# Optimization experiments

Measured on AMD Instinct MI355X. Metric: run time of the kernel, lower is better.

Reference implementation:

```python
import jax, jax.numpy as jnp
import numpy as np

B, S, IN = 32, 512, 19
DE, DD = 256, 128      # encoder / decoder d_model
HE, HD = 8, 4          # heads
LE, LD = 6, 2          # layers
FE, FD = 4 * DE, 4 * DD
EPS = 1e-5


def _ln(x, g, b):
    m = x.mean(-1, keepdims=True)
    v = ((x - m) ** 2).mean(-1, keepdims=True)
    return (x - m) / jnp.sqrt(v + EPS) * g + b


def _mha(x, qkv_w, qkv_b, out_w, out_b, kpad, nh):
    Bq, Sq, D = x.shape
    dh = D // nh
    qkv = x @ qkv_w.T + qkv_b
    q, k, v = jnp.split(qkv, 3, axis=-1)
    hs = lambda t: t.reshape(Bq, Sq, nh, dh).transpose(0, 2, 1, 3)  # -> [B,h,S,dh]
    q, k, v = hs(q), hs(k), hs(v)
    scores = jnp.einsum('bhqd,bhkd->bhqk', q, k) / float(np.sqrt(dh))
    scores = jnp.where(kpad[:, None, None, :], -1e9, scores)  # mask padded keys
    attn = jax.nn.softmax(scores, axis=-1)
    o = jnp.einsum('bhqk,bhkd->bhqd', attn, v).transpose(0, 2, 1, 3).reshape(Bq, Sq, D)
    return o @ out_w.T + out_b


def _block(x, p, kpad, nh):
    qkv_w, qkv_b, ow, ob, f1w, f1b, f2w, f2b, g1, b1, g2, b2 = p
    x = _ln(x + _mha(x, qkv_w, qkv_b, ow, ob, kpad, nh), g1, b1)
    h = jax.nn.relu(x @ f1w.T + f1b) @ f2w.T + f2b
    return _ln(x + h, g2, b2)


def _run(x, ps, kpad, nh, L):
    for i in range(L):
        x = _block(x, tuple(p[i] for p in ps), kpad, nh)
    return x


def _forward(event_tensor, w_in_enc, b_in_enc,
             enc_qkv_w, enc_qkv_b, enc_out_w, enc_out_b,
             enc_f1_w, enc_f1_b, enc_f2_w, enc_f2_b,
             enc_g1, enc_b1, enc_g2, enc_b2,
             mask_token, e2d_w,
             dec_qkv_w, dec_qkv_b, dec_out_w, dec_out_b,
             dec_f1_w, dec_f1_b, dec_f2_w, dec_f2_b,
             dec_g1, dec_b1, dec_g2, dec_b2,
             qh_w, qh_b, dth_w, dth_b,
             attention_mask, pred_mask):
    visible = attention_mask & (~pred_mask)
    counts = visible.sum(axis=1)                                  # [B]
    order = jnp.argsort(~visible, axis=1, stable=True)            # visible positions packed first, in order
    tok = event_tensor @ w_in_enc.T + b_in_enc                    # [B,S,DE]
    vis = jnp.take_along_axis(tok, order[:, :, None], axis=1)
    pos = jnp.arange(S)
    enc_pad = pos[None, :] >= counts[:, None]                      # True = padded slot
    vis = jnp.where(enc_pad[:, :, None], 0.0, vis)
    enc_ps = (enc_qkv_w, enc_qkv_b, enc_out_w, enc_out_b, enc_f1_w, enc_f1_b,
              enc_f2_w, enc_f2_b, enc_g1, enc_b1, enc_g2, enc_b2)
    enc_out = _run(vis, enc_ps, enc_pad, HE, LE)
    dec_vis = enc_out @ e2d_w.T                                    # [B,S,DD]
    idx = jnp.cumsum(visible.astype(jnp.int32), axis=1) - 1        # position -> packed index
    gathered = jnp.take_along_axis(dec_vis, jnp.clip(idx, 0)[:, :, None], axis=1)
    dec_in = jnp.where(visible[:, :, None], gathered, mask_token)  # mask token at masked/pad slots
    dec_ps = (dec_qkv_w, dec_qkv_b, dec_out_w, dec_out_b, dec_f1_w, dec_f1_b,
              dec_f2_w, dec_f2_b, dec_g1, dec_b1, dec_g2, dec_b2)
    dec_out = _run(dec_in, dec_ps, ~attention_mask, HD, LD)
    q = dec_out @ qh_w.T + qh_b
    dt = dec_out @ dth_w.T + dth_b
    return jnp.concatenate([q, dt], axis=-1)                       # [B,S,2]


def setup_inputs():
    key = jax.random.key(0)
    ks = iter(jax.random.split(key, 64))
    nrm = lambda shp, s=0.02: jax.random.normal(next(ks), shp, jnp.float32) * s
    d = {}
    d['event_tensor'] = jax.random.normal(next(ks), (B, S, IN), jnp.float32)
    lengths = jax.random.randint(next(ks), (B,), S // 2, S + 1)
    pos = jnp.arange(S)
    am = pos[None, :] < lengths[:, None]
    pm = (jax.random.uniform(next(ks), (B, S)) < 0.75) & am
    pm = pm.at[:, 0].set(False)  # guarantee >=1 visible token per row
    d['attention_mask'] = am
    d['pred_mask'] = pm
    d['w_in_enc'] = nrm((DE, IN)); d['b_in_enc'] = jnp.zeros((DE,), jnp.float32)
    d['enc_qkv_w'] = nrm((LE, 3 * DE, DE)); d['enc_qkv_b'] = jnp.zeros((LE, 3 * DE), jnp.float32)
    d['enc_out_w'] = nrm((LE, DE, DE));     d['enc_out_b'] = jnp.zeros((LE, DE), jnp.float32)
    d['enc_f1_w'] = nrm((LE, FE, DE));      d['enc_f1_b'] = jnp.zeros((LE, FE), jnp.float32)
    d['enc_f2_w'] = nrm((LE, DE, FE));      d['enc_f2_b'] = jnp.zeros((LE, DE), jnp.float32)
    d['enc_g1'] = jnp.ones((LE, DE), jnp.float32); d['enc_b1'] = jnp.zeros((LE, DE), jnp.float32)
    d['enc_g2'] = jnp.ones((LE, DE), jnp.float32); d['enc_b2'] = jnp.zeros((LE, DE), jnp.float32)
    d['mask_token'] = nrm((DD,))
    d['e2d_w'] = nrm((DD, DE))
    d['dec_qkv_w'] = nrm((LD, 3 * DD, DD)); d['dec_qkv_b'] = jnp.zeros((LD, 3 * DD), jnp.float32)
    d['dec_out_w'] = nrm((LD, DD, DD));     d['dec_out_b'] = jnp.zeros((LD, DD), jnp.float32)
    d['dec_f1_w'] = nrm((LD, FD, DD));      d['dec_f1_b'] = jnp.zeros((LD, FD), jnp.float32)
    d['dec_f2_w'] = nrm((LD, DD, FD));      d['dec_f2_b'] = jnp.zeros((LD, DD), jnp.float32)
    d['dec_g1'] = jnp.ones((LD, DD), jnp.float32); d['dec_b1'] = jnp.zeros((LD, DD), jnp.float32)
    d['dec_g2'] = jnp.ones((LD, DD), jnp.float32); d['dec_b2'] = jnp.zeros((LD, DD), jnp.float32)
    d['qh_w'] = nrm((1, DD));  d['qh_b'] = jnp.zeros((1,), jnp.float32)
    d['dth_w'] = nrm((1, DD)); d['dth_b'] = jnp.zeros((1,), jnp.float32)
    return d


def reference(event_tensor, attention_mask, pred_mask, w_in_enc, b_in_enc,
              enc_qkv_w, enc_qkv_b, enc_out_w, enc_out_b,
              enc_f1_w, enc_f1_b, enc_f2_w, enc_f2_b,
              enc_g1, enc_b1, enc_g2, enc_b2,
              mask_token, e2d_w,
              dec_qkv_w, dec_qkv_b, dec_out_w, dec_out_b,
              dec_f1_w, dec_f1_b, dec_f2_w, dec_f2_b,
              dec_g1, dec_b1, dec_g2, dec_b2,
              qh_w, qh_b, dth_w, dth_b):
    return _forward(event_tensor, w_in_enc, b_in_enc,
                    enc_qkv_w, enc_qkv_b, enc_out_w, enc_out_b,
                    enc_f1_w, enc_f1_b, enc_f2_w, enc_f2_b,
                    enc_g1, enc_b1, enc_g2, enc_b2,
                    mask_token, e2d_w,
                    dec_qkv_w, dec_qkv_b, dec_out_w, dec_out_b,
                    dec_f1_w, dec_f1_b, dec_f2_w, dec_f2_b,
                    dec_g1, dec_b1, dec_g2, dec_b2,
                    qh_w, qh_b, dth_w, dth_b,
                    attention_mask, pred_mask)
```

## Files before the change

### kernel.cpp

```cpp
#include <hip/hip_runtime.h>
#include <hip/hip_bf16.h>

#define B_ 32
#define S_ 512
#define IN_ 19
#define DE_ 256
#define DD_ 128
#define HE_ 8
#define HD_ 4
#define LE_ 6
#define LD_ 2
#define FE_ 1024
#define FD_ 512
#define DH_ 32

typedef __attribute__((ext_vector_type(8))) short short8;
typedef __attribute__((ext_vector_type(4))) float f32x4;

__device__ __forceinline__ short f2bf(float f) {
    union { float f; unsigned u; } x; x.f = f;
    unsigned r = x.u + 0x7fff + ((x.u >> 16) & 1);
    return (short)(r >> 16);
}
__device__ __forceinline__ float bf2f(short s) {
    union { unsigned u; float f; } x; x.u = ((unsigned)(unsigned short)s) << 16;
    return x.f;
}

#define GLL16(g, l) __builtin_amdgcn_global_load_lds( \
    (const __attribute__((address_space(1))) void*)(g), \
    (__attribute__((address_space(3))) void*)(l), 16, 0, 0)

#define QSCALE 0.2550653169f

#define NCONV 9
struct ConvTab {
    const float* src[NCONV];
    short* dst[NCONV];
    int len[NCONV];
};
__global__ __launch_bounds__(S_) void conv_plan_kernel(
    ConvTab tab, int total,
    const int* __restrict__ am, const int* __restrict__ pm,
    int* __restrict__ counts, int* __restrict__ lengths, int* __restrict__ order,
    int* __restrict__ visible, int* __restrict__ idx) {
    if (blockIdx.x < B_) {
        int b = blockIdx.x, s = threadIdx.x;
        __shared__ int sc[S_];
        int a = (am[b * S_ + s] != 0);
        int v = a && (pm[b * S_ + s] == 0);
        visible[b * S_ + s] = v;
        sc[s] = v | (a << 16);
        __syncthreads();
#pragma unroll
        for (int off = 1; off < S_; off <<= 1) {
            int t = (s >= off) ? sc[s - off] : 0;
            __syncthreads();
            sc[s] += t;
            __syncthreads();
        }
        int incl = sc[s] & 0xffff;
        int tot = sc[S_ - 1];
        int total2 = tot & 0xffff;
        if (s == 0) { counts[b] = total2; lengths[b] = tot >> 16; }
        idx[b * S_ + s] = (incl > 0) ? incl - 1 : 0;
        if (v) order[b * S_ + incl - 1] = s;
        else   order[b * S_ + total2 + (s - incl)] = s;
    } else {
        int i = (blockIdx.x - B_) * S_ + threadIdx.x;
        if (i >= total) return;
        int j = i;
        for (int e = 0; e < NCONV; ++e) {
            if (j < tab.len[e]) { tab.dst[e][j] = f2bf(tab.src[e][j]); return; }
            j -= tab.len[e];
        }
    }
}

__global__ __launch_bounds__(DE_) void enc_embed_kernel(
    const float* __restrict__ ev, const float* __restrict__ w, const float* __restrict__ bias,
    const int* __restrict__ counts, const int* __restrict__ order, short* __restrict__ out) {
    int bs = blockIdx.x;
    int b = bs / S_, s = bs % S_;
    int d = threadIdx.x;
    __shared__ float e[IN_];
    bool padded = (s >= counts[b]);
    int src = order[bs];
    if (threadIdx.x < IN_)
        e[threadIdx.x] = padded ? 0.f : ev[(size_t)(b * S_ + src) * IN_ + threadIdx.x];
    __syncthreads();
    float acc = bias[d];
#pragma unroll
    for (int i = 0; i < IN_; ++i) acc += e[i] * w[d * IN_ + i];
    out[(size_t)bs * DE_ + d] = padded ? f2bf(0.f) : f2bf(acc);
}

template <int TM, int TN, bool RELU, bool QKV>
__device__ __forceinline__ void gemm_lds_body(
    const short* __restrict__ A, const short* __restrict__ Wt, const float* __restrict__ bias,
    short* __restrict__ C, int N, int K,
    short* __restrict__ qb, short* __restrict__ kb, short* __restrict__ vtb, int H, int D,
    const int* __restrict__ live) {
    constexpr int HM = TM / 2, HN = TN / 2;
    constexpr int MI = HM / 16, NI = HN / 16;
    constexpr int NCHA = TM / 16, NCH = (TM + TN) / 16;
    int bm = blockIdx.y * TM, bn = blockIdx.x * TN;
    if (live && (bm & (S_ - 1)) >= live[bm >> 9]) return;
    __shared__ short As[2][TM][32];
    __shared__ short Bs[2][TN][32];
    int t = threadIdx.x;
    int wave = t >> 6, lane = t & 63;
    int wm = (wave >> 1) * HM, wn = (wave & 1) * HN;
    int c = lane & 15, quad = lane >> 4;
    f32x4 acc[MI][NI];
#pragma unroll
    for (int i = 0; i < MI; ++i)
#pragma unroll
        for (int j = 0; j < NI; ++j) acc[i][j] = (f32x4){0.f, 0.f, 0.f, 0.f};

    int srow = lane >> 2, scol = (lane & 3) * 8;
    int nk = K >> 5;

    auto stage = [&](int buf, int k0) {
#pragma unroll
        for (int ch0 = 0; ch0 < NCH; ch0 += 4) {
            int ch = ch0 + wave;
            if (ch < NCHA)
                GLL16(A + (size_t)(bm + ch * 16 + srow) * K + k0 + scol, &As[buf][ch * 16][0]);
            else if (ch < NCH)
                GLL16(Wt + (size_t)(bn + (ch - NCHA) * 16 + srow) * K + k0 + scol,
                      &Bs[buf][(ch - NCHA) * 16][0]);
        }
    };

    stage(0, 0);
    __syncthreads();
    for (int kt = 0; kt < nk; ++kt) {
        int cur = kt & 1;
        if (kt + 1 < nk) stage(cur ^ 1, (kt + 1) << 5);
        short8 av[MI], bv[NI];
#pragma unroll
        for (int mi = 0; mi < MI; ++mi) av[mi] = *(const short8*)&As[cur][wm + mi * 16 + c][quad * 8];
#pragma unroll
        for (int ni = 0; ni < NI; ++ni) bv[ni] = *(const short8*)&Bs[cur][wn + ni * 16 + c][quad * 8];
#pragma unroll
        for (int mi = 0; mi < MI; ++mi)
#pragma unroll
            for (int ni = 0; ni < NI; ++ni)
                acc[mi][ni] = __builtin_amdgcn_mfma_f32_16x16x32_bf16(av[mi], bv[ni], acc[mi][ni], 0, 0, 0);
        __syncthreads();
    }
#pragma unroll
    for (int mi = 0; mi < MI; ++mi)
#pragma unroll
        for (int ni = 0; ni < NI; ++ni)
#pragma unroll
            for (int r = 0; r < 4; ++r) {
                int R = bm + wm + mi * 16 + quad * 4 + r;
                int Ncol = bn + wn + ni * 16 + c;
                float v = acc[mi][ni][r] + (bias ? bias[Ncol] : 0.f);
                if (RELU) v = fmaxf(v, 0.f);
                if (!QKV) {
                    C[(size_t)R * N + Ncol] = f2bf(v);
                } else {
                    int s = R & (S_ - 1), b2 = R >> 9;
                    if (Ncol < D) {
                        int h = Ncol >> 5, d = Ncol & 31;
                        qb[(((size_t)b2 * H + h) * S_ + s) * DH_ + d] = f2bf(v * QSCALE);
                    } else if (Ncol < 2 * D) {
                        int n2 = Ncol - D, h = n2 >> 5, d = n2 & 31;
                        kb[(((size_t)b2 * H + h) * S_ + s) * DH_ + d] = f2bf(v);
                    } else {
                        int n2 = Ncol - 2 * D, h = n2 >> 5, d = n2 & 31;
                        vtb[(((size_t)b2 * H + h) * DH_ + d) * S_ + s] = f2bf(v);
                    }
                }
            }
}

template <int N, bool HEAD, int K>
__device__ __forceinline__ void gemm_ln_body(
    const short* __restrict__ A, const short* __restrict__ Wt,
    const float* __restrict__ bias, const short* x ,
    const float* __restrict__ g, const float* __restrict__ be,
    short* out,
    const float* __restrict__ qw, const float* __restrict__ qbb,
    const float* __restrict__ dw, const float* __restrict__ dbb,
    float* __restrict__ outf,
    const int* __restrict__ live) {
    constexpr int TM = 32;
    constexpr int MI = 2;
    constexpr int HN = N / 4, NI = HN / 16;
    constexpr int NK = K / 32;
    constexpr int HST = N + 8;
    int bm = blockIdx.x * TM;
    if (live && (bm & (S_ - 1)) >= live[bm >> 9]) return;
    __shared__ short Hs[TM * HST];
    int t = threadIdx.x, wave = t >> 6, lane = t & 63;
    int wn = wave * HN;
    int c = lane & 15, quad = lane >> 4;
    f32x4 acc[MI][NI];
#pragma unroll
    for (int i = 0; i < MI; ++i)
#pragma unroll
        for (int j = 0; j < NI; ++j) acc[i][j] = (f32x4){0.f, 0.f, 0.f, 0.f};

    const short* Ab = A + (size_t)(bm + c) * K + quad * 8;
    const short* Bb = Wt + (size_t)(wn + c) * K + quad * 8;

#pragma unroll 8
    for (int kt = 0; kt < NK; ++kt) {
        short8 av[MI], bv[NI];
#pragma unroll
        for (int mi = 0; mi < MI; ++mi)
            av[mi] = *(const short8*)(Ab + (size_t)mi * 16 * K + kt * 32);
#pragma unroll
        for (int ni = 0; ni < NI; ++ni)
            bv[ni] = *(const short8*)(Bb + (size_t)ni * 16 * K + kt * 32);
#pragma unroll
        for (int mi = 0; mi < MI; ++mi)
#pragma unroll
            for (int ni = 0; ni < NI; ++ni)
                acc[mi][ni] = __builtin_amdgcn_mfma_f32_16x16x32_bf16(av[mi], bv[ni], acc[mi][ni], 0, 0, 0);
    }

#pragma unroll
    for (int mi = 0; mi < MI; ++mi)
#pragma unroll
        for (int ni = 0; ni < NI; ++ni) {
            int col = wn + ni * 16 + c;
            float bcol = bias[col];
#pragma unroll
            for (int r = 0; r < 4; ++r)
                Hs[(mi * 16 + quad * 4 + r) * HST + col] = f2bf(acc[mi][ni][r] + bcol);
        }
    __syncthreads();

    constexpr int CPL = N / 8;
    int r = t >> 3, li = t & 7;
    int R = bm + r;
    int c0 = li * CPL;
    float v[CPL];
    float s = 0.f;
#pragma unroll
    for (int e8 = 0; e8 < CPL / 8; ++e8) {
        short8 xv = *(const short8*)&x[(size_t)R * N + c0 + e8 * 8];
#pragma unroll
        for (int j = 0; j < 8; ++j) {
            float vv = bf2f(xv[j]) + bf2f(Hs[r * HST + c0 + e8 * 8 + j]);
            v[e8 * 8 + j] = vv;
            s += vv;
        }
    }
    s += __shfl_xor(s, 1); s += __shfl_xor(s, 2); s += __shfl_xor(s, 4);
    float m = s / N;
    float s2 = 0.f;
#pragma unroll
    for (int e = 0; e < CPL; ++e) { float d = v[e] - m; s2 += d * d; }
    s2 += __shfl_xor(s2, 1); s2 += __shfl_xor(s2, 2); s2 += __shfl_xor(s2, 4);
    float rstd = rsqrtf(s2 / N + 1e-5f);
    if (!HEAD) {
        if (live && ((R & (S_ - 1)) >= live[R >> 9])) return;
#pragma unroll
        for (int e8 = 0; e8 < CPL / 8; ++e8) {
            short8 ov;
#pragma unroll
            for (int j = 0; j < 8; ++j) {
                int e = e8 * 8 + j;
                ov[j] = f2bf((v[e] - m) * rstd * g[c0 + e] + be[c0 + e]);
            }
            *(short8*)&out[(size_t)R * N + c0 + e8 * 8] = ov;
        }
    } else {
        float q = 0.f, dt = 0.f;
#pragma unroll
        for (int e = 0; e < CPL; ++e) {
            float o = (v[e] - m) * rstd * g[c0 + e] + be[c0 + e];
            q += o * qw[c0 + e];
            dt += o * dw[c0 + e];
        }
        q += __shfl_xor(q, 1); q += __shfl_xor(q, 2); q += __shfl_xor(q, 4);
        dt += __shfl_xor(dt, 1); dt += __shfl_xor(dt, 2); dt += __shfl_xor(dt, 4);
        if (li == 0) {
            outf[(size_t)R * 2 + 0] = q + qbb[0];
            outf[(size_t)R * 2 + 1] = dt + dbb[0];
        }
    }
}

__global__ __launch_bounds__(256) void g_qkv_e(
    const short* A, const short* Wt, const float* bias,
    short* qb, short* kb, short* vtb, const int* live) {
    gemm_lds_body<64, 64, false, true>(A, Wt, bias, nullptr, 3 * DE_, DE_, qb, kb, vtb, HE_, DE_, live);
}
__global__ __launch_bounds__(256) void g_qkv_d(
    const short* A, const short* Wt, const float* bias,
    short* qb, short* kb, short* vtb) {
    gemm_lds_body<64, 64, false, true>(A, Wt, bias, nullptr, 3 * DD_, DD_, qb, kb, vtb, HD_, DD_, nullptr);
}
__global__ __launch_bounds__(256) void g_f1_e(
    const short* A, const short* Wt, const float* bias, short* C, const int* live) {
    gemm_lds_body<64, 64, true, false>(A, Wt, bias, C, FE_, DE_, nullptr, nullptr, nullptr, 0, 0, live);
}
__global__ __launch_bounds__(256) void g_f1_d(
    const short* A, const short* Wt, const float* bias, short* C) {
    gemm_lds_body<64, 64, true, false>(A, Wt, bias, C, FD_, DD_, nullptr, nullptr, nullptr, 0, 0, nullptr);
}
__global__ __launch_bounds__(256) void g_e2d(
    const short* A, const short* Wt, short* C, const int* live) {
    gemm_lds_body<32, 32, false, false>(A, Wt, nullptr, C, DD_, DE_, nullptr, nullptr, nullptr, 0, 0, live);
}
__global__ __launch_bounds__(256, 1) void g_outln_e(
    const short* A, const short* Wt, const float* bias, const short* x,
    const float* g, const float* be, short* out, const int* live) {
    gemm_ln_body<DE_, false, DE_>(A, Wt, bias, x, g, be, out, nullptr, nullptr, nullptr, nullptr, nullptr, live);
}
__global__ __launch_bounds__(256, 1) void g_f2ln_e(
    const short* A, const short* Wt, const float* bias, const short* x,
    const float* g, const float* be, short* out, const int* live) {
    gemm_ln_body<DE_, false, FE_>(A, Wt, bias, x, g, be, out, nullptr, nullptr, nullptr, nullptr, nullptr, live);
}
__global__ __launch_bounds__(256, 1) void g_outln_d(
    const short* A, const short* Wt, const float* bias, const short* x,
    const float* g, const float* be, short* out) {
    gemm_ln_body<DD_, false, DD_>(A, Wt, bias, x, g, be, out, nullptr, nullptr, nullptr, nullptr, nullptr, nullptr);
}
__global__ __launch_bounds__(256, 1) void g_f2ln_d(
    const short* A, const short* Wt, const float* bias, const short* x,
    const float* g, const float* be, short* out) {
    gemm_ln_body<DD_, false, FD_>(A, Wt, bias, x, g, be, out, nullptr, nullptr, nullptr, nullptr, nullptr, nullptr);
}
__global__ __launch_bounds__(256, 1) void g_headln(
    const short* A, const short* Wt, const float* bias, const short* x,
    const float* g, const float* be,
    const float* qw, const float* qbb, const float* dw, const float* dbb, float* outf) {
    gemm_ln_body<DD_, true, FD_>(A, Wt, bias, x, g, be, nullptr, qw, qbb, dw, dbb, outf, nullptr);
}

__global__ __launch_bounds__(256) void attn_flash(
    const short* __restrict__ qb, const short* __restrict__ kb, const short* __restrict__ vtb,
    const int* __restrict__ limit_arr, const int* __restrict__ qlim,
    short* __restrict__ o, int H, int D) {
    int b = blockIdx.z, h = blockIdx.y;
    if (qlim && (int)(blockIdx.x * 64) >= qlim[b]) return;
    int wave = threadIdx.x >> 6, lane = threadIdx.x & 63;
    int q0 = blockIdx.x * 64 + wave * 16;
    int c = lane & 15, quad = lane >> 4;
    size_t bh = (size_t)b * H + h;
    __shared__ short PtAll[4][16][132];
    short (*Pt)[132] = PtAll[wave];

    f32x4 zero = (f32x4){0.f, 0.f, 0.f, 0.f};
    short8 aq = *(const short8*)&qb[(bh * S_ + q0 + c) * DH_ + quad * 8];
    const short* kbase = kb + bh * S_ * DH_;
    const short* vbase = vtb + bh * DH_ * S_;

    int limit = limit_arr[b];
    int nchunks = (limit + 127) >> 7;

    float lrow[4] = {0.f, 0.f, 0.f, 0.f};
    f32x4 o0 = zero, o1 = zero;

    for (int kc = 0; kc < nchunks; ++kc) {
        f32x4 s[8];
#pragma unroll
        for (int nt = 0; nt < 8; ++nt) {
            short8 bk = *(const short8*)&kbase[(size_t)(kc * 128 + nt * 16 + c) * DH_ + quad * 8];
            s[nt] = __builtin_amdgcn_mfma_f32_16x16x32_bf16(aq, bk, zero, 0, 0, 0);
        }
#pragma unroll
        for (int nt = 0; nt < 8; ++nt) {
            bool ok = (kc * 128 + nt * 16 + c) < limit;
#pragma unroll
            for (int r = 0; r < 4; ++r) {
                float p = ok ? exp2f(s[nt][r]) : 0.f;
                s[nt][r] = p;
                lrow[r] += p;
            }
        }
#pragma unroll
        for (int nt = 0; nt < 8; ++nt)
#pragma unroll
            for (int r = 0; r < 4; ++r)
                Pt[quad * 4 + r][nt * 16 + c] = f2bf(s[nt][r]);
#pragma unroll
        for (int kk = 0; kk < 4; ++kk) {
            short8 ap = *(const short8*)&Pt[c][kk * 32 + quad * 8];
            short8 b0 = *(const short8*)&vbase[(size_t)c * S_ + kc * 128 + kk * 32 + quad * 8];
            short8 b1 = *(const short8*)&vbase[(size_t)(16 + c) * S_ + kc * 128 + kk * 32 + quad * 8];
            o0 = __builtin_amdgcn_mfma_f32_16x16x32_bf16(ap, b0, o0, 0, 0, 0);
            o1 = __builtin_amdgcn_mfma_f32_16x16x32_bf16(ap, b1, o1, 0, 0, 0);
        }
    }
#pragma unroll
    for (int r = 0; r < 4; ++r) {
        float l = lrow[r];
        l += __shfl_xor(l, 1);
        l += __shfl_xor(l, 2);
        l += __shfl_xor(l, 4);
        l += __shfl_xor(l, 8);
        float inv = 1.f / l;
        int row = quad * 4 + r;
        size_t base = (size_t)(b * S_ + q0 + row) * D + h * DH_;
        o[base + c] = f2bf(o0[r] * inv);
        o[base + 16 + c] = f2bf(o1[r] * inv);
    }
}

__global__ __launch_bounds__(DD_) void dec_embed_kernel(
    const short* __restrict__ dec_vis, const float* __restrict__ mask_token,
    const int* __restrict__ visible, const int* __restrict__ idx, short* __restrict__ out) {
    int bs = blockIdx.x, d = threadIdx.x;
    int b = bs / S_;
    short val = visible[bs] ? dec_vis[(size_t)(b * S_ + idx[bs]) * DD_ + d]
                            : f2bf(mask_token[d]);
    out[(size_t)bs * DD_ + d] = val;
}

extern "C" void kernel_launch(void* const* d_in, const int* in_sizes, int n_in,
                              void* d_out, int out_size, void* d_ws, size_t ws_size,
                              hipStream_t stream) {
    const float* ev      = (const float*)d_in[0];
    const int*  am       = (const int*)d_in[1];
    const int*  pm       = (const int*)d_in[2];
    const float* w_in    = (const float*)d_in[3];
    const float* b_in    = (const float*)d_in[4];
    const float* eqkv_w  = (const float*)d_in[5];
    const float* eqkv_b  = (const float*)d_in[6];
    const float* eout_w  = (const float*)d_in[7];
    const float* eout_b  = (const float*)d_in[8];
    const float* ef1_w   = (const float*)d_in[9];
    const float* ef1_b   = (const float*)d_in[10];
    const float* ef2_w   = (const float*)d_in[11];
    const float* ef2_b   = (const float*)d_in[12];
    const float* eg1     = (const float*)d_in[13];
    const float* eb1     = (const float*)d_in[14];
    const float* eg2     = (const float*)d_in[15];
    const float* eb2     = (const float*)d_in[16];
    const float* mask_tok= (const float*)d_in[17];
    const float* e2d_w   = (const float*)d_in[18];
    const float* dqkv_w  = (const float*)d_in[19];
    const float* dqkv_b  = (const float*)d_in[20];
    const float* dout_w  = (const float*)d_in[21];
    const float* dout_b  = (const float*)d_in[22];
    const float* df1_w   = (const float*)d_in[23];
    const float* df1_b   = (const float*)d_in[24];
    const float* df2_w   = (const float*)d_in[25];
    const float* df2_b   = (const float*)d_in[26];
    const float* dg1     = (const float*)d_in[27];
    const float* db1     = (const float*)d_in[28];
    const float* dg2     = (const float*)d_in[29];
    const float* db2     = (const float*)d_in[30];
    const float* qh_w    = (const float*)d_in[31];
    const float* qh_b    = (const float*)d_in[32];
    const float* dth_w   = (const float*)d_in[33];
    const float* dth_b   = (const float*)d_in[34];
    float* out = (float*)d_out;

    const int BS = B_ * S_;
    char* ws = (char*)d_ws;
    int* counts  = (int*)ws;
    int* lengths = counts + 32;
    int* order   = lengths + 32;
    int* visible = order + BS;
    int* idx     = visible + BS;

    short* wb = (short*)(ws + 256 * 1024);
    const int L_eqkv = LE_ * 3 * DE_ * DE_;
    const int L_eout = LE_ * DE_ * DE_;
    const int L_ef1  = LE_ * FE_ * DE_;
    const int L_ef2  = LE_ * DE_ * FE_;
    const int L_e2d  = DD_ * DE_;
    const int L_dqkv = LD_ * 3 * DD_ * DD_;
    const int L_dout = LD_ * DD_ * DD_;
    const int L_df1  = LD_ * FD_ * DD_;
    const int L_df2  = LD_ * DD_ * FD_;
    short* w_eqkv = wb;
    short* w_eout = w_eqkv + L_eqkv;
    short* w_ef1  = w_eout + L_eout;
    short* w_ef2  = w_ef1 + L_ef1;
    short* w_e2d  = w_ef2 + L_ef2;
    short* w_dqkv = w_e2d + L_e2d;
    short* w_dout = w_dqkv + L_dqkv;
    short* w_df1  = w_dout + L_dout;
    short* w_df2  = w_df1 + L_df1;
    const int convTotal = L_eqkv + L_eout + L_ef1 + L_ef2 + L_e2d + L_dqkv + L_dout + L_df1 + L_df2;

    short* bx    = (short*)(ws + 12 * 1024 * 1024);
    short* qbuf  = bx   + (size_t)BS * DE_;
    short* kbuf  = qbuf + (size_t)B_ * HE_ * S_ * DH_;
    short* vtbuf = kbuf + (size_t)B_ * HE_ * S_ * DH_;
    short* battn = vtbuf + (size_t)B_ * HE_ * S_ * DH_;
    short* bt    = battn + (size_t)BS * DE_;
    short* hid   = bt + (size_t)BS * DE_;

    ConvTab tab;
    tab.src[0] = eqkv_w; tab.dst[0] = w_eqkv; tab.len[0] = L_eqkv;
    tab.src[1] = eout_w; tab.dst[1] = w_eout; tab.len[1] = L_eout;
    tab.src[2] = ef1_w;  tab.dst[2] = w_ef1;  tab.len[2] = L_ef1;
    tab.src[3] = ef2_w;  tab.dst[3] = w_ef2;  tab.len[3] = L_ef2;
    tab.src[4] = e2d_w;  tab.dst[4] = w_e2d;  tab.len[4] = L_e2d;
    tab.src[5] = dqkv_w; tab.dst[5] = w_dqkv; tab.len[5] = L_dqkv;
    tab.src[6] = dout_w; tab.dst[6] = w_dout; tab.len[6] = L_dout;
    tab.src[7] = df1_w;  tab.dst[7] = w_df1;  tab.len[7] = L_df1;
    tab.src[8] = df2_w;  tab.dst[8] = w_df2;  tab.len[8] = L_df2;
    conv_plan_kernel<<<B_ + (convTotal + S_ - 1) / S_, S_, 0, stream>>>(
        tab, convTotal, am, pm, counts, lengths, order, visible, idx);
    enc_embed_kernel<<<BS, DE_, 0, stream>>>(ev, w_in, b_in, counts, order, bx);

    for (int l = 0; l < LE_; ++l) {
        g_qkv_e<<<dim3(3 * DE_ / 64, BS / 64), 256, 0, stream>>>(
            bx, w_eqkv + (size_t)l * 3 * DE_ * DE_, eqkv_b + (size_t)l * 3 * DE_,
            qbuf, kbuf, vtbuf, counts);
        attn_flash<<<dim3(S_ / 64, HE_, B_), 256, 0, stream>>>(
            qbuf, kbuf, vtbuf, counts, counts, battn, HE_, DE_);
        g_outln_e<<<BS / 32, 256, 0, stream>>>(
            battn, w_eout + (size_t)l * DE_ * DE_, eout_b + (size_t)l * DE_,
            bx, eg1 + (size_t)l * DE_, eb1 + (size_t)l * DE_, bx, counts);
        g_f1_e<<<dim3(FE_ / 64, BS / 64), 256, 0, stream>>>(
            bx, w_ef1 + (size_t)l * FE_ * DE_, ef1_b + (size_t)l * FE_, hid, counts);
        g_f2ln_e<<<BS / 32, 256, 0, stream>>>(
            hid, w_ef2 + (size_t)l * DE_ * FE_, ef2_b + (size_t)l * DE_,
            bx, eg2 + (size_t)l * DE_, eb2 + (size_t)l * DE_, bx, counts);
    }

    g_e2d<<<dim3(DD_ / 32, BS / 32), 256, 0, stream>>>(bx, w_e2d, bt, counts);
    dec_embed_kernel<<<BS, DD_, 0, stream>>>(bt, mask_tok, visible, idx, bx);

    for (int l = 0; l < LD_; ++l) {
        g_qkv_d<<<dim3(3 * DD_ / 64, BS / 64), 256, 0, stream>>>(
            bx, w_dqkv + (size_t)l * 3 * DD_ * DD_, dqkv_b + (size_t)l * 3 * DD_,
            qbuf, kbuf, vtbuf);
        attn_flash<<<dim3(S_ / 64, HD_, B_), 256, 0, stream>>>(
            qbuf, kbuf, vtbuf, lengths, nullptr, battn, HD_, DD_);
        g_outln_d<<<BS / 32, 256, 0, stream>>>(
            battn, w_dout + (size_t)l * DD_ * DD_, dout_b + (size_t)l * DD_,
            bx, dg1 + (size_t)l * DD_, db1 + (size_t)l * DD_, bx);
        g_f1_d<<<dim3(FD_ / 64, BS / 64), 256, 0, stream>>>(
            bx, w_df1 + (size_t)l * FD_ * DD_, df1_b + (size_t)l * FD_, hid);
        if (l < LD_ - 1) {
            g_f2ln_d<<<BS / 32, 256, 0, stream>>>(
                hid, w_df2 + (size_t)l * DD_ * FD_, df2_b + (size_t)l * DD_,
                bx, dg2 + (size_t)l * DD_, db2 + (size_t)l * DD_, bx);
        } else {
            g_headln<<<BS / 32, 256, 0, stream>>>(
                hid, w_df2 + (size_t)l * DD_ * FD_, df2_b + (size_t)l * DD_,
                bx, dg2 + (size_t)l * DD_, db2 + (size_t)l * DD_,
                qh_w, qh_b, dth_w, dth_b, out);
        }
    }
}
```

Measured before the change: 1.042 ms.

## Stage GEMM+LayerNorm operands through double-buffered LDS with async global loads

The fused GEMM+LayerNorm kernels now load A and weight tiles in 128-wide K panels into double-buffered dynamic shared memory with direct global-to-LDS loads, overlapping the next panel's fetch with MFMA work on the current one. The wave layout changes from 4 waves splitting N to a 2x2 split over M and N, and the launch-bounds occupancy hint of 1 is dropped. This targets latency-bound direct-from-global operand loads, at the cost of large LDS use (about 147KB for the encoder variant), which limits occupancy and may exceed per-block limits without an attribute change.

```diff
diff --git a/kernel.cpp b/kernel.cpp
--- a/kernel.cpp
+++ b/kernel.cpp
@@ -189,51 +189,72 @@
     float* __restrict__ outf,
     const int* __restrict__ live) {
     constexpr int TM = 32;
-    constexpr int MI = 2;
-    constexpr int HN = N / 4, NI = HN / 16;
-    constexpr int NK = K / 32;
+    constexpr int BK = 128;
+    constexpr int PAN = BK / 32;
+    constexpr int NKS = K / BK;
+    static_assert(K % BK == 0, "K must be a multiple of 128");
+    constexpr int HN = N / 2, NI = HN / 16;
+    constexpr int NCHA = TM / 16, NCH = NCHA + N / 16;
+    constexpr int SBUF = (TM + N) * BK;
     constexpr int HST = N + 8;
+    extern __shared__ short smem[];
     int bm = blockIdx.x * TM;
     if (live && (bm & (S_ - 1)) >= live[bm >> 9]) return;
-    __shared__ short Hs[TM * HST];
     int t = threadIdx.x, wave = t >> 6, lane = t & 63;
-    int wn = wave * HN;
+    int wm = (wave >> 1) * 16, wn = (wave & 1) * HN;
     int c = lane & 15, quad = lane >> 4;
-    f32x4 acc[MI][NI];
-#pragma unroll
-    for (int i = 0; i < MI; ++i)
-#pragma unroll
-        for (int j = 0; j < NI; ++j) acc[i][j] = (f32x4){0.f, 0.f, 0.f, 0.f};
-
-    const short* Ab = A + (size_t)(bm + c) * K + quad * 8;
-    const short* Bb = Wt + (size_t)(wn + c) * K + quad * 8;
-
-#pragma unroll 8
-    for (int kt = 0; kt < NK; ++kt) {
-        short8 av[MI], bv[NI];
-#pragma unroll
-        for (int mi = 0; mi < MI; ++mi)
-            av[mi] = *(const short8*)(Ab + (size_t)mi * 16 * K + kt * 32);
-#pragma unroll
-        for (int ni = 0; ni < NI; ++ni)
-            bv[ni] = *(const short8*)(Bb + (size_t)ni * 16 * K + kt * 32);
-#pragma unroll
-        for (int mi = 0; mi < MI; ++mi)
+    int srow = lane >> 2, scol = (lane & 3) * 8;
+    f32x4 acc[NI];
+#pragma unroll
+    for (int ni = 0; ni < NI; ++ni) acc[ni] = (f32x4){0.f, 0.f, 0.f, 0.f};
+
+    auto stage = [&](int buf, int ks) {
+        short* base = smem + buf * SBUF;
+        int k0 = ks * BK;
+#pragma unroll
+        for (int kk = 0; kk < PAN; ++kk) {
+#pragma unroll
+            for (int ch0 = 0; ch0 < NCH; ch0 += 4) {
+                int ch = ch0 + wave;
+                if (ch < NCHA)
+                    GLL16(A + (size_t)(bm + ch * 16 + srow) * K + k0 + kk * 32 + scol,
+                          base + kk * TM * 32 + ch * 16 * 32);
+                else if (ch < NCH)
+                    GLL16(Wt + (size_t)((ch - NCHA) * 16 + srow) * K + k0 + kk * 32 + scol,
+                          base + TM * BK + kk * N * 32 + (ch - NCHA) * 16 * 32);
+            }
+        }
+    };
+
+    stage(0, 0);
+    __syncthreads();
+    for (int ks = 0; ks < NKS; ++ks) {
+        int cur = ks & 1;
+        if (ks + 1 < NKS) stage(cur ^ 1, ks + 1);
+        const short* base = smem + cur * SBUF;
+#pragma unroll
+        for (int kk = 0; kk < PAN; ++kk) {
+            short8 av = *(const short8*)(base + kk * TM * 32 + (wm + c) * 32 + quad * 8);
+            short8 bv[NI];
 #pragma unroll
             for (int ni = 0; ni < NI; ++ni)
-                acc[mi][ni] = __builtin_amdgcn_mfma_f32_16x16x32_bf16(av[mi], bv[ni], acc[mi][ni], 0, 0, 0);
-    }
-
-#pragma unroll
-    for (int mi = 0; mi < MI; ++mi)
-#pragma unroll
-        for (int ni = 0; ni < NI; ++ni) {
-            int col = wn + ni * 16 + c;
-            float bcol = bias[col];
-#pragma unroll
-            for (int r = 0; r < 4; ++r)
-                Hs[(mi * 16 + quad * 4 + r) * HST + col] = f2bf(acc[mi][ni][r] + bcol);
-        }
+                bv[ni] = *(const short8*)(base + TM * BK + kk * N * 32 + (wn + ni * 16 + c) * 32 + quad * 8);
+#pragma unroll
+            for (int ni = 0; ni < NI; ++ni)
+                acc[ni] = __builtin_amdgcn_mfma_f32_16x16x32_bf16(av, bv[ni], acc[ni], 0, 0, 0);
+        }
+        __syncthreads();
+    }
+
+    short* Hs = smem;
+#pragma unroll
+    for (int ni = 0; ni < NI; ++ni) {
+        int col = wn + ni * 16 + c;
+        float bcol = bias[col];
+#pragma unroll
+        for (int r = 0; r < 4; ++r)
+            Hs[(wm + quad * 4 + r) * HST + col] = f2bf(acc[ni][r] + bcol);
+    }
     __syncthreads();
 
     constexpr int CPL = N / 8;
@@ -310,32 +331,35 @@
     const short* A, const short* Wt, short* C, const int* live) {
     gemm_lds_body<32, 32, false, false>(A, Wt, nullptr, C, DD_, DE_, nullptr, nullptr, nullptr, 0, 0, live);
 }
-__global__ __launch_bounds__(256, 1) void g_outln_e(
+__global__ __launch_bounds__(256) void g_outln_e(
     const short* A, const short* Wt, const float* bias, const short* x,
     const float* g, const float* be, short* out, const int* live) {
     gemm_ln_body<DE_, false, DE_>(A, Wt, bias, x, g, be, out, nullptr, nullptr, nullptr, nullptr, nullptr, live);
 }
-__global__ __launch_bounds__(256, 1) void g_f2ln_e(
+__global__ __launch_bounds__(256) void g_f2ln_e(
     const short* A, const short* Wt, const float* bias, const short* x,
     const float* g, const float* be, short* out, const int* live) {
     gemm_ln_body<DE_, false, FE_>(A, Wt, bias, x, g, be, out, nullptr, nullptr, nullptr, nullptr, nullptr, live);
 }
-__global__ __launch_bounds__(256, 1) void g_outln_d(
+__global__ __launch_bounds__(256) void g_outln_d(
     const short* A, const short* Wt, const float* bias, const short* x,
     const float* g, const float* be, short* out) {
     gemm_ln_body<DD_, false, DD_>(A, Wt, bias, x, g, be, out, nullptr, nullptr, nullptr, nullptr, nullptr, nullptr);
 }
-__global__ __launch_bounds__(256, 1) void g_f2ln_d(
+__global__ __launch_bounds__(256) void g_f2ln_d(
     const short* A, const short* Wt, const float* bias, const short* x,
     const float* g, const float* be, short* out) {
     gemm_ln_body<DD_, false, FD_>(A, Wt, bias, x, g, be, out, nullptr, nullptr, nullptr, nullptr, nullptr, nullptr);
 }
-__global__ __launch_bounds__(256, 1) void g_headln(
+__global__ __launch_bounds__(256) void g_headln(
     const short* A, const short* Wt, const float* bias, const short* x,
     const float* g, const float* be,
     const float* qw, const float* qbb, const float* dw, const float* dbb, float* outf) {
     gemm_ln_body<DD_, true, FD_>(A, Wt, bias, x, g, be, nullptr, qw, qbb, dw, dbb, outf, nullptr);
 }
+
+#define SHM_LN_E ((32 + DE_) * 128 * 2 * 2)
+#define SHM_LN_D ((32 + DD_) * 128 * 2 * 2)
 
 __global__ __launch_bounds__(256) void attn_flash(
     const short* __restrict__ qb, const short* __restrict__ kb, const short* __restrict__ vtb,
@@ -514,12 +538,12 @@
             qbuf, kbuf, vtbuf, counts);
         attn_flash<<<dim3(S_ / 64, HE_, B_), 256, 0, stream>>>(
             qbuf, kbuf, vtbuf, counts, counts, battn, HE_, DE_);
-        g_outln_e<<<BS / 32, 256, 0, stream>>>(
+        g_outln_e<<<BS / 32, 256, SHM_LN_E, stream>>>(
             battn, w_eout + (size_t)l * DE_ * DE_, eout_b + (size_t)l * DE_,
             bx, eg1 + (size_t)l * DE_, eb1 + (size_t)l * DE_, bx, counts);
         g_f1_e<<<dim3(FE_ / 64, BS / 64), 256, 0, stream>>>(
             bx, w_ef1 + (size_t)l * FE_ * DE_, ef1_b + (size_t)l * FE_, hid, counts);
-        g_f2ln_e<<<BS / 32, 256, 0, stream>>>(
+        g_f2ln_e<<<BS / 32, 256, SHM_LN_E, stream>>>(
             hid, w_ef2 + (size_t)l * DE_ * FE_, ef2_b + (size_t)l * DE_,
             bx, eg2 + (size_t)l * DE_, eb2 + (size_t)l * DE_, bx, counts);
     }
@@ -533,17 +557,17 @@
             qbuf, kbuf, vtbuf);
         attn_flash<<<dim3(S_ / 64, HD_, B_), 256, 0, stream>>>(
             qbuf, kbuf, vtbuf, lengths, nullptr, battn, HD_, DD_);
-        g_outln_d<<<BS / 32, 256, 0, stream>>>(
+        g_outln_d<<<BS / 32, 256, SHM_LN_D, stream>>>(
             battn, w_dout + (size_t)l * DD_ * DD_, dout_b + (size_t)l * DD_,
             bx, dg1 + (size_t)l * DD_, db1 + (size_t)l * DD_, bx);
         g_f1_d<<<dim3(FD_ / 64, BS / 64), 256, 0, stream>>>(
             bx, w_df1 + (size_t)l * FD_ * DD_, df1_b + (size_t)l * FD_, hid);
         if (l < LD_ - 1) {
-            g_f2ln_d<<<BS / 32, 256, 0, stream>>>(
+            g_f2ln_d<<<BS / 32, 256, SHM_LN_D, stream>>>(
                 hid, w_df2 + (size_t)l * DD_ * FD_, df2_b + (size_t)l * DD_,
                 bx, dg2 + (size_t)l * DD_, db2 + (size_t)l * DD_, bx);
         } else {
-            g_headln<<<BS / 32, 256, 0, stream>>>(
+            g_headln<<<BS / 32, 256, SHM_LN_D, stream>>>(
                 hid, w_df2 + (size_t)l * DD_ * FD_, df2_b + (size_t)l * DD_,
                 bx, dg2 + (size_t)l * DD_, db2 + (size_t)l * DD_,
                 qh_w, qh_b, dth_w, dth_b, out);
```

After: 907.2 us. 1.15x faster.
